# Kernel tuning notes

Hardware: AMD Instinct MI355X
Metric: run time of the kernel (lower is better)

Reference implementation:

```python
import jax, jax.numpy as jnp
import numpy as np
import math

# Dims (match torchaudio Emformer config in init_kwargs)
B, U, D = 4, 512, 80
H, FFN, L = 8, 2048, 12
SEG, LC, RC = 32, 50, 8            # segment_length, left_context, right_context
NUM_SEGS = math.ceil(U / SEG)
RC_LEN = RC * NUM_SEGS
K = RC_LEN + U                      # query/key length = [hard-copied right-context blocks, utterance]
OUT_DIM = 768
EPS = 1e-5
SCALE = (D // H) ** -0.5

def _rc_indices():
    # torchaudio _gen_right_context: per segment, copy the next RC frames; last block is input[T-RC:]
    T = U + RC
    idx = []
    for i in range(NUM_SEGS - 1):
        s = (i + 1) * SEG
        idx.extend(range(s, s + RC))
    idx.extend(range(T - RC, T))
    return np.asarray(idx)

def _attention_mask():
    # torchaudio _gen_attention_mask with use_mem=False. True = disallowed.
    # Rows: all RC blocks (NUM_SEGS * RC rows) first, then utterance queries per segment.
    rc_rows, q_rows = [], []
    for i in range(NUM_SEGS):
        allowed = np.zeros(K, dtype=bool)
        allowed[i * RC:(i + 1) * RC] = True                       # own right-context block
        s = max(i * SEG - LC, 0)
        e = min((i + 1) * SEG, U)
        allowed[RC_LEN + s:RC_LEN + e] = True                     # segment + left context
        rc_rows.append(np.tile(allowed, (RC, 1)))
        q_rows.append(np.tile(allowed, (min(SEG, U - i * SEG), 1)))
    return ~np.concatenate(rc_rows + q_rows, axis=0)              # (K, K)

RC_IDX = _rc_indices()
ATT_MASK = _attention_mask()

def _layer_norm(x, g, b):
    m = jnp.mean(x, axis=-1, keepdims=True)
    v = jnp.var(x, axis=-1, keepdims=True)
    return (x - m) * jax.lax.rsqrt(v + EPS) * g + b

def setup_inputs() -> dict:
    key = jax.random.key(0)
    ks = jax.random.split(key, 8)
    w = lambda k, *s: jax.random.normal(k, s, jnp.float32) * 0.02
    return {
        "mel_input": jax.random.normal(ks[0], (B, U + RC, D), jnp.float32),
        "ln_in_g": jnp.ones((L, D)), "ln_in_b": jnp.zeros((L, D)),
        "Wq": w(ks[1], L, D, D), "bq": jnp.zeros((L, D)),
        "Wkv": w(ks[2], L, 2 * D, D), "bkv": jnp.zeros((L, 2 * D)),
        "Wo": w(ks[3], L, D, D), "bo": jnp.zeros((L, D)),
        "ln_ff_g": jnp.ones((L, D)), "ln_ff_b": jnp.zeros((L, D)),
        "W1": w(ks[4], L, FFN, D), "b1": jnp.zeros((L, FFN)),
        "W2": w(ks[5], L, D, FFN), "b2": jnp.zeros((L, D)),
        "ln_out_g": jnp.ones((L, D)), "ln_out_b": jnp.zeros((L, D)),
        "Wp": w(ks[6], OUT_DIM, D), "bp": jnp.zeros((OUT_DIM,)),
        "lengths": jnp.full((B,), U, dtype=jnp.int32),
    }

def _emformer(mel_input, ln_in_g, ln_in_b, Wq, bq, Wkv, bkv, Wo, bo,
              ln_ff_g, ln_ff_b, W1, b1, W2, b2, ln_out_g, ln_out_b, Wp, bp, lengths):
    att_mask = jnp.asarray(ATT_MASK)
    utt = mel_input[:, :U]                       # (B, U, D)
    rc = mel_input[:, jnp.asarray(RC_IDX)]       # (B, RC_LEN, D)
    # key padding mask over [rc, utterance]: key positions >= lengths + RC_LEN are padded (negative_inf = -1e8)
    pad_mask = jnp.arange(K)[None, :] >= (lengths + RC_LEN)[:, None]   # (B, K)

    def layer(carry, p):
        (lg, lb, wq, bq_, wkv, bkv_, wo, bo_, fg, fb, w1, b1_, w2, b2_, og, ob) = p
        utt, rc = carry
        x = jnp.concatenate([rc, utt], axis=1)   # (B, K, D) -- torchaudio cats [right_context, utterance]
        ln = _layer_norm(x, lg, lb)              # pre-attention LayerNorm
        q = (ln @ wq.T + bq_).reshape(B, K, H, D // H)
        k_, v_ = jnp.split(ln @ wkv.T + bkv_, 2, axis=-1)
        k_ = k_.reshape(B, K, H, D // H)
        v_ = v_.reshape(B, K, H, D // H)
        s = jnp.einsum('bqhd,bkhd->bhqk', q * SCALE, k_).astype(jnp.float32)
        s = jnp.where(att_mask[None, None], -jnp.inf, s)
        s = jnp.where(pad_mask[:, None, None, :], -1e8, s)
        a = jax.nn.softmax(s, axis=-1).astype(x.dtype)
        attn = jnp.einsum('bhqk,bkhd->bqhd', a, v_).reshape(B, K, D)
        res = attn @ wo.T + bo_ + x              # residual with pre-LN input
        ff = _layer_norm(res, fg, fb)            # pos_ff: LN -> Linear -> ReLU -> Linear
        ff = jax.nn.relu(ff @ w1.T + b1_) @ w2.T + b2_
        res = _layer_norm(res + ff, og, ob)      # post LayerNorm
        return (res[:, RC_LEN:], res[:, :RC_LEN]), None

    xs = (ln_in_g, ln_in_b, Wq, bq, Wkv, bkv, Wo, bo, ln_ff_g, ln_ff_b, W1, b1, W2, b2, ln_out_g, ln_out_b)
    (utt, rc), _ = jax.lax.scan(layer, (utt, rc), xs)
    return utt @ Wp.T + bp                       # final projection 80 -> 768

def reference(mel_input, ln_in_g, ln_in_b, Wq, bq, Wkv, bkv, Wo, bo,
              ln_ff_g, ln_ff_b, W1, b1, W2, b2, ln_out_g, ln_out_b, Wp, bp, lengths):
    out = _emformer(mel_input, ln_in_g, ln_in_b, Wq, bq, Wkv, bkv, Wo, bo,
                    ln_ff_g, ln_ff_b, W1, b1, W2, b2, ln_out_g, ln_out_b, Wp, bp, lengths)
    return out, lengths
```

## Files before the change

### kernel.cpp

```cpp
#include <hip/hip_runtime.h>
#include <math.h>

#define BB 4
#define UU 512
#define DD 80
#define HH 8
#define FFND 2048
#define LL 12
#define SEGC 32
#define LCC 50
#define RCC 8
#define NSEG 16
#define RCL 128
#define KK 640
#define ROWS (BB*KK)
#define OUTD 768
#define NSPLIT 8
#define EPSF 1e-5f
#define SCALEF 0.31622776601683794f

typedef __attribute__((ext_vector_type(8))) short bf16x8;
typedef __attribute__((ext_vector_type(4))) float f32x4;

__device__ inline unsigned short f2bf(float f) {
  unsigned int u = __float_as_uint(f);
  u += 0x7fffu + ((u >> 16) & 1u);
  return (unsigned short)(u >> 16);
}

__global__ __launch_bounds__(256) void k_gather(const float* __restrict__ mel,
                                                float* __restrict__ x) {
  int idx = blockIdx.x * 256 + threadIdx.x;
  if (idx >= ROWS * DD) return;
  int d = idx % DD;
  int row = idx / DD;
  int b = row / KK;
  int j = row % KK;
  int pos;
  if (j < RCL) {
    int i = j >> 3, r = j & 7;
    pos = (i < NSEG - 1) ? (i + 1) * SEGC + r : UU + r;
  } else {
    pos = j - RCL;
  }
  x[idx] = mel[(b * (UU + RCC) + pos) * DD + d];
}

__global__ __launch_bounds__(256) void k_cvt(const float* __restrict__ W1,
                                             const float* __restrict__ W2,
                                             unsigned short* __restrict__ o1,
                                             unsigned short* __restrict__ o2) {
  const int NV = (LL * FFND * DD) / 4;
  int t = blockIdx.x * 256 + threadIdx.x;
  const float* src;
  unsigned short* dst;
  int i;
  if (t < NV) { src = W1; dst = o1; i = t; }
  else        { src = W2; dst = o2; i = t - NV; }
  float4 v = reinterpret_cast<const float4*>(src)[i];
  ushort4 r;
  r.x = f2bf(v.x); r.y = f2bf(v.y); r.z = f2bf(v.z); r.w = f2bf(v.w);
  reinterpret_cast<ushort4*>(dst)[i] = r;
}

__global__ __launch_bounds__(256) void k_qkv(
    const float* __restrict__ x, float* __restrict__ qkv,
    const float* __restrict__ Wq, const float* __restrict__ bq,
    const float* __restrict__ Wkv, const float* __restrict__ bkv,
    const float* __restrict__ lg, const float* __restrict__ lb) {
  __shared__ float s_x[32 * 84];
  __shared__ float s_w[80 * 84];
  __shared__ float s_mu[32], s_ri[32];
  int tid = threadIdx.x;
  int r0 = blockIdx.x * 32;
  int ct = blockIdx.y;
  for (int k = 0; k < 3; ++k) {
    int idx = tid + k * 256;
    if (idx < 640) {
      int row = idx / 20, c4 = idx % 20;
      *reinterpret_cast<float4*>(&s_x[row * 84 + c4 * 4]) =
          *reinterpret_cast<const float4*>(&x[(r0 + row) * DD + c4 * 4]);
    }
  }
  const float* Wbase = (ct == 0) ? Wq : (ct == 1 ? Wkv : (Wkv + 80 * DD));
  for (int k = 0; k < 7; ++k) {
    int idx = tid + k * 256;
    if (idx < 1600) {
      int c = idx / 20, d4 = idx % 20;
      *reinterpret_cast<float4*>(&s_w[c * 84 + d4 * 4]) =
          *reinterpret_cast<const float4*>(&Wbase[c * DD + d4 * 4]);
    }
  }
  __syncthreads();
  {
    int rr = tid >> 3, t8 = tid & 7;
    float sm = 0.f, sq = 0.f;
    for (int d = t8 * 10; d < t8 * 10 + 10; ++d) {
      float v = s_x[rr * 84 + d];
      sm += v; sq += v * v;
    }
    for (int m = 4; m >= 1; m >>= 1) {
      sm += __shfl_xor(sm, m, 8);
      sq += __shfl_xor(sq, m, 8);
    }
    if (t8 == 0) {
      float mu = sm * (1.f / DD);
      float var = sq * (1.f / DD) - mu * mu;
      s_mu[rr] = mu;
      s_ri[rr] = rsqrtf(var + EPSF);
    }
  }
  __syncthreads();
  for (int k = 0; k < 10; ++k) {
    int e = tid + k * 256;
    int row = e / 80, d = e % 80;
    s_x[row * 84 + d] = (s_x[row * 84 + d] - s_mu[row]) * s_ri[row] * lg[d] + lb[d];
  }
  __syncthreads();
  int ty = tid >> 4, tx = tid & 15;
  float acc[2][5] = {};
  for (int d4 = 0; d4 < 20; ++d4) {
    float4 a0 = *reinterpret_cast<const float4*>(&s_x[(2 * ty) * 84 + d4 * 4]);
    float4 a1 = *reinterpret_cast<const float4*>(&s_x[(2 * ty + 1) * 84 + d4 * 4]);
#pragma unroll
    for (int j = 0; j < 5; ++j) {
      float4 w = *reinterpret_cast<const float4*>(&s_w[(tx + 16 * j) * 84 + d4 * 4]);
      acc[0][j] += a0.x * w.x + a0.y * w.y + a0.z * w.z + a0.w * w.w;
      acc[1][j] += a1.x * w.x + a1.y * w.y + a1.z * w.z + a1.w * w.w;
    }
  }
  const float* bias = (ct == 0) ? bq : (bkv + (ct == 2 ? 80 : 0));
  for (int i2 = 0; i2 < 2; ++i2)
    for (int j = 0; j < 5; ++j) {
      int c = tx + 16 * j;
      int grow = r0 + 2 * ty + i2;
      qkv[grow * 240 + ct * 80 + c] = acc[i2][j] + bias[c];
    }
}

__global__ __launch_bounds__(256) void k_attn(const float* __restrict__ qkv,
                                              float* __restrict__ attn,
                                              const int* __restrict__ lengths) {
  int i = blockIdx.x, h = blockIdx.y, b = blockIdx.z;
  int tid = threadIdx.x;
  int s = i * SEGC - LCC; if (s < 0) s = 0;
  int e = (i + 1) * SEGC;
  int nk = RCC + (e - s);
  __shared__ float s_k[90 * 10], s_v[90 * 10], s_q[40 * 10];
  __shared__ float s_p[40 * 90], s_kb[90], s_den[40];
  int len = lengths[b];
  if (tid < 90 && tid < nk) {
    int j = tid;
    int kr = (j < RCC) ? i * RCC + j : RCL + s + (j - RCC);
    const float* kp = &qkv[(b * KK + kr) * 240 + 80 + h * 10];
    const float* vp = &qkv[(b * KK + kr) * 240 + 160 + h * 10];
#pragma unroll
    for (int d = 0; d < 10; ++d) { s_k[j * 10 + d] = kp[d]; s_v[j * 10 + d] = vp[d]; }
    s_kb[j] = (kr >= len + RCL) ? -1e8f : 0.f;
  }
  if (tid >= 128 && tid < 168) {
    int j = tid - 128;
    int qr = (j < RCC) ? i * RCC + j : RCL + i * SEGC + (j - RCC);
    const float* qp = &qkv[(b * KK + qr) * 240 + h * 10];
#pragma unroll
    for (int d = 0; d < 10; ++d) s_q[j * 10 + d] = qp[d];
  }
  __syncthreads();
  for (int p = tid; p < 3600; p += 256) {
    int q = p / 90, jk = p % 90;
    float sc = -1e30f;
    if (jk < nk) {
      float dot = 0.f;
#pragma unroll
      for (int d = 0; d < 10; ++d) dot += s_q[q * 10 + d] * s_k[jk * 10 + d];
      sc = dot * SCALEF + s_kb[jk];
    }
    s_p[p] = sc;
  }
  __syncthreads();
  if (tid < 160) {
    int r = tid >> 2, l4 = tid & 3;
    float m = -1e30f;
    for (int kx = l4; kx < 90; kx += 4) m = fmaxf(m, s_p[r * 90 + kx]);
    m = fmaxf(m, __shfl_xor(m, 1, 4));
    m = fmaxf(m, __shfl_xor(m, 2, 4));
    float sum = 0.f;
    for (int kx = l4; kx < 90; kx += 4) {
      float ev = __expf(s_p[r * 90 + kx] - m);
      s_p[r * 90 + kx] = ev;
      sum += ev;
    }
    sum += __shfl_xor(sum, 1, 4);
    sum += __shfl_xor(sum, 2, 4);
    if (l4 == 0) s_den[r] = sum;
  }
  __syncthreads();
  for (int po = tid; po < 400; po += 256) {
    int q = po / 10, d = po % 10;
    float o = 0.f;
    for (int kx = 0; kx < 90; ++kx) o += s_p[q * 90 + kx] * s_v[kx * 10 + d];
    int qr = (q < RCC) ? i * RCC + q : RCL + i * SEGC + (q - RCC);
    attn[(b * KK + qr) * DD + h * 10 + d] = o / s_den[q];
  }
}

__global__ __launch_bounds__(256) void k_oproj(
    const float* __restrict__ attn, const float* __restrict__ Wo,
    const float* __restrict__ bo, const float* __restrict__ x,
    float* __restrict__ res, unsigned short* __restrict__ ffln_bf,
    const float* __restrict__ fg, const float* __restrict__ fb) {
  __shared__ float s_at[16 * 84], s_x2[16 * 84], s_wo[80 * 84];
  int tid = threadIdx.x;
  int r0 = blockIdx.x * 16;
  for (int k = 0; k < 2; ++k) {
    int idx = tid + k * 256;
    if (idx < 320) {
      int row = idx / 20, c4 = idx % 20;
      *reinterpret_cast<float4*>(&s_at[row * 84 + c4 * 4]) =
          *reinterpret_cast<const float4*>(&attn[(r0 + row) * DD + c4 * 4]);
      *reinterpret_cast<float4*>(&s_x2[row * 84 + c4 * 4]) =
          *reinterpret_cast<const float4*>(&x[(r0 + row) * DD + c4 * 4]);
    }
  }
  for (int k = 0; k < 7; ++k) {
    int idx = tid + k * 256;
    if (idx < 1600) {
      int c = idx / 20, d4 = idx % 20;
      *reinterpret_cast<float4*>(&s_wo[c * 84 + d4 * 4]) =
          *reinterpret_cast<const float4*>(&Wo[c * DD + d4 * 4]);
    }
  }
  __syncthreads();
  int r = tid >> 4, tx = tid & 15;
  float acc[5] = {};
  for (int d4 = 0; d4 < 20; ++d4) {
    float4 a = *reinterpret_cast<const float4*>(&s_at[r * 84 + d4 * 4]);
#pragma unroll
    for (int j = 0; j < 5; ++j) {
      float4 w = *reinterpret_cast<const float4*>(&s_wo[(tx + 16 * j) * 84 + d4 * 4]);
      acc[j] += a.x * w.x + a.y * w.y + a.z * w.z + a.w * w.w;
    }
  }
  float val[5];
  float sm = 0.f, sq = 0.f;
#pragma unroll
  for (int j = 0; j < 5; ++j) {
    int c = tx + 16 * j;
    float v = acc[j] + bo[c] + s_x2[r * 84 + c];
    val[j] = v;
    res[(r0 + r) * DD + c] = v;
    sm += v; sq += v * v;
  }
  for (int m = 8; m >= 1; m >>= 1) {
    sm += __shfl_xor(sm, m, 16);
    sq += __shfl_xor(sq, m, 16);
  }
  float mu = sm * (1.f / DD);
  float ri = rsqrtf(sq * (1.f / DD) - mu * mu + EPSF);
#pragma unroll
  for (int j = 0; j < 5; ++j) {
    int c = tx + 16 * j;
    ffln_bf[(r0 + r) * DD + c] = f2bf((val[j] - mu) * ri * fg[c] + fb[c]);
  }
}

__global__ __launch_bounds__(256) void k_ffn(
    const unsigned short* __restrict__ A, const unsigned short* __restrict__ W1,
    const float* __restrict__ b1, const unsigned short* __restrict__ W2,
    float* __restrict__ part) {
  __shared__ unsigned short s_a[64 * 104];
  __shared__ unsigned short s_w1[128 * 104];
  __shared__ unsigned short s_h[64 * 136];
  __shared__ unsigned short s_w2[80 * 136];
  int tid = threadIdx.x;
  int r0 = blockIdx.x * 64;
  int F0 = blockIdx.y * 256;
  int w = tid >> 6, lane = tid & 63;
  int m = lane & 15, q = lane >> 4;

  for (int k = 0; k < 3; ++k) {
    int idx = tid + k * 256;
    if (idx < 640) {
      int row = idx / 10, ch = idx % 10;
      *reinterpret_cast<uint4*>(&s_a[row * 104 + ch * 8]) =
          *reinterpret_cast<const uint4*>(&A[(r0 + row) * DD + ch * 8]);
    }
  }
  if (tid < 128) {
    int row = tid >> 1, half = tid & 1;
    uint4 z = make_uint4(0, 0, 0, 0);
    *reinterpret_cast<uint4*>(&s_a[row * 104 + 80 + half * 8]) = z;
  }
  {
    int fc0 = F0;
    for (int k = 0; k < 5; ++k) {
      int idx = tid + k * 256;
      int row = idx / 10, ch = idx % 10;
      *reinterpret_cast<uint4*>(&s_w1[row * 104 + ch * 8]) =
          *reinterpret_cast<const uint4*>(&W1[(fc0 + row) * DD + ch * 8]);
    }
    {
      int row = tid >> 1, half = tid & 1;
      uint4 z = make_uint4(0, 0, 0, 0);
      *reinterpret_cast<uint4*>(&s_w1[row * 104 + 80 + half * 8]) = z;
    }
    for (int k = 0; k < 5; ++k) {
      int idx = tid + k * 256;
      int row = idx >> 4, ch = idx & 15;
      *reinterpret_cast<uint4*>(&s_w2[row * 136 + ch * 8]) =
          *reinterpret_cast<const uint4*>(&W2[row * FFND + fc0 + ch * 8]);
    }
  }
  __syncthreads();

  f32x4 acc2[5] = {};
  for (int c = 0; c < 2; ++c) {
    int fc0 = F0 + c * 128;
    f32x4 acc1[8] = {};
#pragma unroll
    for (int kk = 0; kk < 3; ++kk) {
      bf16x8 a = *reinterpret_cast<const bf16x8*>(&s_a[(w * 16 + m) * 104 + kk * 32 + q * 8]);
#pragma unroll
      for (int ct = 0; ct < 8; ++ct) {
        bf16x8 b = *reinterpret_cast<const bf16x8*>(&s_w1[(ct * 16 + m) * 104 + kk * 32 + q * 8]);
        acc1[ct] = __builtin_amdgcn_mfma_f32_16x16x32_bf16(a, b, acc1[ct], 0, 0, 0);
      }
    }
#pragma unroll
    for (int ct = 0; ct < 8; ++ct) {
      int col = ct * 16 + m;
      float bias = b1[fc0 + col];
#pragma unroll
      for (int r = 0; r < 4; ++r) {
        int row = w * 16 + q * 4 + r;
        s_h[row * 136 + col] = f2bf(fmaxf(acc1[ct][r] + bias, 0.f));
      }
    }
    __syncthreads();
#pragma unroll
    for (int kk = 0; kk < 4; ++kk) {
      bf16x8 a = *reinterpret_cast<const bf16x8*>(&s_h[(w * 16 + m) * 136 + kk * 32 + q * 8]);
#pragma unroll
      for (int ct = 0; ct < 5; ++ct) {
        bf16x8 b = *reinterpret_cast<const bf16x8*>(&s_w2[(ct * 16 + m) * 136 + kk * 32 + q * 8]);
        acc2[ct] = __builtin_amdgcn_mfma_f32_16x16x32_bf16(a, b, acc2[ct], 0, 0, 0);
      }
    }
    __syncthreads();
    if (c == 0) {
      int fn = F0 + 128;
      for (int k = 0; k < 5; ++k) {
        int idx = tid + k * 256;
        int row = idx / 10, ch = idx % 10;
        *reinterpret_cast<uint4*>(&s_w1[row * 104 + ch * 8]) =
            *reinterpret_cast<const uint4*>(&W1[(fn + row) * DD + ch * 8]);
      }
      for (int k = 0; k < 5; ++k) {
        int idx = tid + k * 256;
        int row = idx >> 4, ch = idx & 15;
        *reinterpret_cast<uint4*>(&s_w2[row * 136 + ch * 8]) =
            *reinterpret_cast<const uint4*>(&W2[row * FFND + fn + ch * 8]);
      }
      __syncthreads();
    }
  }
#pragma unroll
  for (int ct = 0; ct < 5; ++ct)
#pragma unroll
    for (int r = 0; r < 4; ++r) {
      int grow = r0 + w * 16 + q * 4 + r;
      part[blockIdx.y * (ROWS * DD) + grow * DD + ct * 16 + m] = acc2[ct][r];
    }
}

__global__ __launch_bounds__(128) void k_comb(
    const float* __restrict__ part, const float* __restrict__ b2,
    const float* __restrict__ res, float* __restrict__ x,
    const float* __restrict__ og, const float* __restrict__ ob) {
  int row = blockIdx.x;
  int t = threadIdx.x;
  __shared__ float rsum[128], rsq[128];
  float v = 0.f;
  if (t < DD) {
#pragma unroll
    for (int s = 0; s < NSPLIT; ++s) v += part[s * (ROWS * DD) + row * DD + t];
    v += b2[t] + res[row * DD + t];
  }
  rsum[t] = (t < DD) ? v : 0.f;
  rsq[t] = (t < DD) ? v * v : 0.f;
  __syncthreads();
  for (int m2 = 64; m2 >= 1; m2 >>= 1) {
    if (t < m2) { rsum[t] += rsum[t + m2]; rsq[t] += rsq[t + m2]; }
    __syncthreads();
  }
  float mu = rsum[0] * (1.f / DD);
  float ri = rsqrtf(rsq[0] * (1.f / DD) - mu * mu + EPSF);
  if (t < DD) x[row * DD + t] = (v - mu) * ri * og[t] + ob[t];
}

__global__ __launch_bounds__(256) void k_proj(
    const float* __restrict__ x, const float* __restrict__ Wp,
    const float* __restrict__ bp, const int* __restrict__ lengths,
    float* __restrict__ out) {
  __shared__ float s_a[64 * 84], s_w[64 * 84];
  int tid = threadIdx.x;
  int gr0 = blockIdx.x * 64;
  int c0 = blockIdx.y * 64;
  int b = gr0 / UU;
  int u0 = gr0 % UU;
  for (int k = 0; k < 5; ++k) {
    int idx = tid + k * 256;
    int row = idx / 20, c4 = idx % 20;
    *reinterpret_cast<float4*>(&s_a[row * 84 + c4 * 4]) =
        *reinterpret_cast<const float4*>(&x[(b * KK + RCL + u0 + row) * DD + c4 * 4]);
    *reinterpret_cast<float4*>(&s_w[row * 84 + c4 * 4]) =
        *reinterpret_cast<const float4*>(&Wp[(c0 + row) * DD + c4 * 4]);
  }
  __syncthreads();
  int ty = tid >> 4, tx = tid & 15;
  float acc[4][4] = {};
  for (int d4 = 0; d4 < 20; ++d4) {
    float4 a[4], w[4];
#pragma unroll
    for (int i2 = 0; i2 < 4; ++i2)
      a[i2] = *reinterpret_cast<const float4*>(&s_a[(4 * ty + i2) * 84 + d4 * 4]);
#pragma unroll
    for (int j = 0; j < 4; ++j)
      w[j] = *reinterpret_cast<const float4*>(&s_w[(tx + 16 * j) * 84 + d4 * 4]);
#pragma unroll
    for (int i2 = 0; i2 < 4; ++i2)
#pragma unroll
      for (int j = 0; j < 4; ++j)
        acc[i2][j] += a[i2].x * w[j].x + a[i2].y * w[j].y +
                      a[i2].z * w[j].z + a[i2].w * w[j].w;
  }
  for (int i2 = 0; i2 < 4; ++i2)
    for (int j = 0; j < 4; ++j) {
      int c = c0 + tx + 16 * j;
      out[(gr0 + 4 * ty + i2) * OUTD + c] = acc[i2][j] + bp[c];
    }
  if (blockIdx.x == 0 && blockIdx.y == 0 && tid < BB)
    out[BB * UU * OUTD + tid] = (float)lengths[tid];
}

extern "C" void kernel_launch(void* const* d_in, const int* in_sizes, int n_in,
                              void* d_out, int out_size, void* d_ws, size_t ws_size,
                              hipStream_t stream) {
  const float* mel   = (const float*)d_in[0];
  const float* lng   = (const float*)d_in[1];
  const float* lnb   = (const float*)d_in[2];
  const float* Wq    = (const float*)d_in[3];
  const float* bq    = (const float*)d_in[4];
  const float* Wkv   = (const float*)d_in[5];
  const float* bkv   = (const float*)d_in[6];
  const float* Wo    = (const float*)d_in[7];
  const float* bo    = (const float*)d_in[8];
  const float* ffg   = (const float*)d_in[9];
  const float* ffb   = (const float*)d_in[10];
  const float* W1    = (const float*)d_in[11];
  const float* b1    = (const float*)d_in[12];
  const float* W2    = (const float*)d_in[13];
  const float* b2    = (const float*)d_in[14];
  const float* og    = (const float*)d_in[15];
  const float* ob    = (const float*)d_in[16];
  const float* Wp    = (const float*)d_in[17];
  const float* bp    = (const float*)d_in[18];
  const int*   lens  = (const int*)d_in[19];
  float* out = (float*)d_out;

  float* ws   = (float*)d_ws;
  float* x    = ws;
  float* qkv  = x + ROWS * DD;
  float* part = qkv;
  float* attn = qkv + NSPLIT * ROWS * DD;
  float* res  = attn + ROWS * DD;
  unsigned short* ffln_bf = (unsigned short*)(res + ROWS * DD);
  unsigned short* w1bf    = ffln_bf + ROWS * DD;
  unsigned short* w2bf    = w1bf + LL * FFND * DD;

  k_gather<<<(ROWS * DD + 255) / 256, 256, 0, stream>>>(mel, x);
  k_cvt<<<(2 * (LL * FFND * DD) / 4 + 255) / 256, 256, 0, stream>>>(W1, W2, w1bf, w2bf);

  for (int l = 0; l < LL; ++l) {
    const float* lWq  = Wq  + l * DD * DD;
    const float* lbq  = bq  + l * DD;
    const float* lWkv = Wkv + l * 2 * DD * DD;
    const float* lbkv = bkv + l * 2 * DD;
    const float* lWo  = Wo  + l * DD * DD;
    const float* lbo  = bo  + l * DD;
    const unsigned short* lW1 = w1bf + l * FFND * DD;
    const float* lb1  = b1  + l * FFND;
    const unsigned short* lW2 = w2bf + l * FFND * DD;
    const float* lb2  = b2  + l * DD;

    k_qkv<<<dim3(ROWS / 32, 3), 256, 0, stream>>>(
        x, qkv, lWq, lbq, lWkv, lbkv, lng + l * DD, lnb + l * DD);
    k_attn<<<dim3(NSEG, HH, BB), 256, 0, stream>>>(qkv, attn, lens);
    k_oproj<<<ROWS / 16, 256, 0, stream>>>(
        attn, lWo, lbo, x, res, ffln_bf, ffg + l * DD, ffb + l * DD);
    k_ffn<<<dim3(ROWS / 64, NSPLIT), 256, 0, stream>>>(ffln_bf, lW1, lb1, lW2, part);
    k_comb<<<ROWS, 128, 0, stream>>>(part, lb2, res, x, og + l * DD, ob + l * DD);
  }

  k_proj<<<dim3(BB * UU / 64, OUTD / 64), 256, 0, stream>>>(x, Wp, bp, lens, out);
}
```

Before: 616.9 us.

## Fuse attention with output projection and fold FFN combine into next-layer QKV

Attention and the output projection now run in one kernel: each block handles one segment and batch for all heads and keeps the attention output in shared memory, so the separate attn buffer round trip is gone. The FFN split-sum, bias, residual and post-LayerNorm step is folded into the next layer's QKV kernel, and for the last layer into the final projection kernel. This cuts per-layer launches from five to three. In exchange, the attention grid shrinks from 512 small blocks to 64 large blocks with about 110KB of LDS each, and each thread loops serially over four heads, which lowers parallelism in that stage.

```diff
diff --git a/kernel.cpp b/kernel.cpp
--- a/kernel.cpp
+++ b/kernel.cpp
@@ -63,25 +63,21 @@
   reinterpret_cast<ushort4*>(dst)[i] = r;
 }
 
-__global__ __launch_bounds__(256) void k_qkv(
-    const float* __restrict__ x, float* __restrict__ qkv,
+__global__ __launch_bounds__(256) void k_qkvcomb(
+    const float* __restrict__ xin, float* __restrict__ xout,
+    float* __restrict__ qkv,
     const float* __restrict__ Wq, const float* __restrict__ bq,
     const float* __restrict__ Wkv, const float* __restrict__ bkv,
-    const float* __restrict__ lg, const float* __restrict__ lb) {
+    const float* __restrict__ lg, const float* __restrict__ lb,
+    const float* __restrict__ part, const float* __restrict__ res,
+    const float* __restrict__ pb2, const float* __restrict__ pog,
+    const float* __restrict__ pob, int use_comb) {
   __shared__ float s_x[32 * 84];
   __shared__ float s_w[80 * 84];
   __shared__ float s_mu[32], s_ri[32];
   int tid = threadIdx.x;
   int r0 = blockIdx.x * 32;
   int ct = blockIdx.y;
-  for (int k = 0; k < 3; ++k) {
-    int idx = tid + k * 256;
-    if (idx < 640) {
-      int row = idx / 20, c4 = idx % 20;
-      *reinterpret_cast<float4*>(&s_x[row * 84 + c4 * 4]) =
-          *reinterpret_cast<const float4*>(&x[(r0 + row) * DD + c4 * 4]);
-    }
-  }
   const float* Wbase = (ct == 0) ? Wq : (ct == 1 ? Wkv : (Wkv + 80 * DD));
   for (int k = 0; k < 7; ++k) {
     int idx = tid + k * 256;
@@ -91,7 +87,54 @@
           *reinterpret_cast<const float4*>(&Wbase[c * DD + d4 * 4]);
     }
   }
-  __syncthreads();
+  if (!use_comb) {
+    for (int k = 0; k < 3; ++k) {
+      int idx = tid + k * 256;
+      if (idx < 640) {
+        int row = idx / 20, c4 = idx % 20;
+        *reinterpret_cast<float4*>(&s_x[row * 84 + c4 * 4]) =
+            *reinterpret_cast<const float4*>(&xin[(r0 + row) * DD + c4 * 4]);
+      }
+    }
+    __syncthreads();
+  } else {
+    for (int k = 0; k < 10; ++k) {
+      int idx = tid + k * 256;
+      int row = idx / 80, c = idx % 80;
+      int g = r0 + row;
+      float v = pb2[c] + res[g * DD + c];
+#pragma unroll
+      for (int s5 = 0; s5 < NSPLIT; ++s5) v += part[s5 * (ROWS * DD) + g * DD + c];
+      s_x[row * 84 + c] = v;
+    }
+    __syncthreads();
+    {
+      int rr = tid >> 3, t8 = tid & 7;
+      float sm = 0.f, sq = 0.f;
+      for (int d = t8 * 10; d < t8 * 10 + 10; ++d) {
+        float v = s_x[rr * 84 + d];
+        sm += v; sq += v * v;
+      }
+      for (int m = 4; m >= 1; m >>= 1) {
+        sm += __shfl_xor(sm, m, 8);
+        sq += __shfl_xor(sq, m, 8);
+      }
+      if (t8 == 0) {
+        float mu = sm * (1.f / DD);
+        s_mu[rr] = mu;
+        s_ri[rr] = rsqrtf(sq * (1.f / DD) - mu * mu + EPSF);
+      }
+    }
+    __syncthreads();
+    for (int k = 0; k < 10; ++k) {
+      int e = tid + k * 256;
+      int row = e / 80, d = e % 80;
+      float xv = (s_x[row * 84 + d] - s_mu[row]) * s_ri[row] * pog[d] + pob[d];
+      s_x[row * 84 + d] = xv;
+      if (ct == 0) xout[(r0 + row) * DD + d] = xv;
+    }
+    __syncthreads();
+  }
   {
     int rr = tid >> 3, t8 = tid & 7;
     float sm = 0.f, sq = 0.f;
@@ -105,9 +148,8 @@
     }
     if (t8 == 0) {
       float mu = sm * (1.f / DD);
-      float var = sq * (1.f / DD) - mu * mu;
       s_mu[rr] = mu;
-      s_ri[rr] = rsqrtf(var + EPSF);
+      s_ri[rr] = rsqrtf(sq * (1.f / DD) - mu * mu + EPSF);
     }
   }
   __syncthreads();
@@ -138,129 +180,143 @@
     }
 }
 
-__global__ __launch_bounds__(256) void k_attn(const float* __restrict__ qkv,
-                                              float* __restrict__ attn,
-                                              const int* __restrict__ lengths) {
-  int i = blockIdx.x, h = blockIdx.y, b = blockIdx.z;
+__global__ __launch_bounds__(512) void k_attnoproj(
+    const float* __restrict__ qkv, const float* __restrict__ x,
+    const float* __restrict__ Wo, const float* __restrict__ bo,
+    float* __restrict__ res, unsigned short* __restrict__ ffln_bf,
+    const float* __restrict__ fg, const float* __restrict__ fb,
+    const int* __restrict__ lengths) {
+  int i = blockIdx.x, b = blockIdx.y;
   int tid = threadIdx.x;
+  __shared__ float s_k[90 * 80], s_v[90 * 80], s_q[40 * 80];
+  __shared__ float s_ao[40 * 84], s_wo[80 * 84], s_kb[90];
   int s = i * SEGC - LCC; if (s < 0) s = 0;
   int e = (i + 1) * SEGC;
   int nk = RCC + (e - s);
-  __shared__ float s_k[90 * 10], s_v[90 * 10], s_q[40 * 10];
-  __shared__ float s_p[40 * 90], s_kb[90], s_den[40];
   int len = lengths[b];
-  if (tid < 90 && tid < nk) {
-    int j = tid;
+  for (int idx = tid; idx < nk * 20; idx += 512) {
+    int j = idx / 20, c4 = idx % 20;
     int kr = (j < RCC) ? i * RCC + j : RCL + s + (j - RCC);
-    const float* kp = &qkv[(b * KK + kr) * 240 + 80 + h * 10];
-    const float* vp = &qkv[(b * KK + kr) * 240 + 160 + h * 10];
-#pragma unroll
-    for (int d = 0; d < 10; ++d) { s_k[j * 10 + d] = kp[d]; s_v[j * 10 + d] = vp[d]; }
-    s_kb[j] = (kr >= len + RCL) ? -1e8f : 0.f;
-  }
-  if (tid >= 128 && tid < 168) {
-    int j = tid - 128;
+    const float* bp_ = &qkv[(b * KK + kr) * 240];
+    *reinterpret_cast<float4*>(&s_k[j * 80 + c4 * 4]) =
+        *reinterpret_cast<const float4*>(bp_ + 80 + c4 * 4);
+    *reinterpret_cast<float4*>(&s_v[j * 80 + c4 * 4]) =
+        *reinterpret_cast<const float4*>(bp_ + 160 + c4 * 4);
+  }
+  if (tid < 90) {
+    float kb = 0.f;
+    if (tid < nk) {
+      int kr = (tid < RCC) ? i * RCC + tid : RCL + s + (tid - RCC);
+      kb = (kr >= len + RCL) ? -1e8f : 0.f;
+    }
+    s_kb[tid] = kb;
+  }
+  for (int idx = tid; idx < 800; idx += 512) {
+    int j = idx / 20, c4 = idx % 20;
     int qr = (j < RCC) ? i * RCC + j : RCL + i * SEGC + (j - RCC);
-    const float* qp = &qkv[(b * KK + qr) * 240 + h * 10];
-#pragma unroll
-    for (int d = 0; d < 10; ++d) s_q[j * 10 + d] = qp[d];
-  }
-  __syncthreads();
-  for (int p = tid; p < 3600; p += 256) {
-    int q = p / 90, jk = p % 90;
-    float sc = -1e30f;
-    if (jk < nk) {
-      float dot = 0.f;
-#pragma unroll
-      for (int d = 0; d < 10; ++d) dot += s_q[q * 10 + d] * s_k[jk * 10 + d];
-      sc = dot * SCALEF + s_kb[jk];
-    }
-    s_p[p] = sc;
-  }
-  __syncthreads();
-  if (tid < 160) {
-    int r = tid >> 2, l4 = tid & 3;
-    float m = -1e30f;
-    for (int kx = l4; kx < 90; kx += 4) m = fmaxf(m, s_p[r * 90 + kx]);
-    m = fmaxf(m, __shfl_xor(m, 1, 4));
-    m = fmaxf(m, __shfl_xor(m, 2, 4));
-    float sum = 0.f;
-    for (int kx = l4; kx < 90; kx += 4) {
-      float ev = __expf(s_p[r * 90 + kx] - m);
-      s_p[r * 90 + kx] = ev;
-      sum += ev;
-    }
-    sum += __shfl_xor(sum, 1, 4);
-    sum += __shfl_xor(sum, 2, 4);
-    if (l4 == 0) s_den[r] = sum;
-  }
-  __syncthreads();
-  for (int po = tid; po < 400; po += 256) {
-    int q = po / 10, d = po % 10;
-    float o = 0.f;
-    for (int kx = 0; kx < 90; ++kx) o += s_p[q * 90 + kx] * s_v[kx * 10 + d];
-    int qr = (q < RCC) ? i * RCC + q : RCL + i * SEGC + (q - RCC);
-    attn[(b * KK + qr) * DD + h * 10 + d] = o / s_den[q];
-  }
-}
-
-__global__ __launch_bounds__(256) void k_oproj(
-    const float* __restrict__ attn, const float* __restrict__ Wo,
-    const float* __restrict__ bo, const float* __restrict__ x,
-    float* __restrict__ res, unsigned short* __restrict__ ffln_bf,
-    const float* __restrict__ fg, const float* __restrict__ fb) {
-  __shared__ float s_at[16 * 84], s_x2[16 * 84], s_wo[80 * 84];
-  int tid = threadIdx.x;
-  int r0 = blockIdx.x * 16;
-  for (int k = 0; k < 2; ++k) {
-    int idx = tid + k * 256;
-    if (idx < 320) {
-      int row = idx / 20, c4 = idx % 20;
-      *reinterpret_cast<float4*>(&s_at[row * 84 + c4 * 4]) =
-          *reinterpret_cast<const float4*>(&attn[(r0 + row) * DD + c4 * 4]);
-      *reinterpret_cast<float4*>(&s_x2[row * 84 + c4 * 4]) =
-          *reinterpret_cast<const float4*>(&x[(r0 + row) * DD + c4 * 4]);
-    }
-  }
-  for (int k = 0; k < 7; ++k) {
-    int idx = tid + k * 256;
-    if (idx < 1600) {
-      int c = idx / 20, d4 = idx % 20;
-      *reinterpret_cast<float4*>(&s_wo[c * 84 + d4 * 4]) =
-          *reinterpret_cast<const float4*>(&Wo[c * DD + d4 * 4]);
-    }
-  }
-  __syncthreads();
-  int r = tid >> 4, tx = tid & 15;
-  float acc[5] = {};
-  for (int d4 = 0; d4 < 20; ++d4) {
-    float4 a = *reinterpret_cast<const float4*>(&s_at[r * 84 + d4 * 4]);
-#pragma unroll
-    for (int j = 0; j < 5; ++j) {
-      float4 w = *reinterpret_cast<const float4*>(&s_wo[(tx + 16 * j) * 84 + d4 * 4]);
-      acc[j] += a.x * w.x + a.y * w.y + a.z * w.z + a.w * w.w;
-    }
-  }
-  float val[5];
-  float sm = 0.f, sq = 0.f;
-#pragma unroll
-  for (int j = 0; j < 5; ++j) {
-    int c = tx + 16 * j;
-    float v = acc[j] + bo[c] + s_x2[r * 84 + c];
-    val[j] = v;
-    res[(r0 + r) * DD + c] = v;
-    sm += v; sq += v * v;
-  }
-  for (int m = 8; m >= 1; m >>= 1) {
-    sm += __shfl_xor(sm, m, 16);
-    sq += __shfl_xor(sq, m, 16);
-  }
-  float mu = sm * (1.f / DD);
-  float ri = rsqrtf(sq * (1.f / DD) - mu * mu + EPSF);
-#pragma unroll
-  for (int j = 0; j < 5; ++j) {
-    int c = tx + 16 * j;
-    ffln_bf[(r0 + r) * DD + c] = f2bf((val[j] - mu) * ri * fg[c] + fb[c]);
+    *reinterpret_cast<float4*>(&s_q[j * 80 + c4 * 4]) =
+        *reinterpret_cast<const float4*>(&qkv[(b * KK + qr) * 240 + c4 * 4]);
+  }
+  for (int idx = tid; idx < 1600; idx += 512) {
+    int c = idx / 20, d4 = idx % 20;
+    *reinterpret_cast<float4*>(&s_wo[c * 84 + d4 * 4]) =
+        *reinterpret_cast<const float4*>(&Wo[c * DD + d4 * 4]);
+  }
+  __syncthreads();
+  int hg = tid >> 8;
+  int t2 = tid & 255;
+  int q = t2 >> 2, l4 = t2 & 3;
+  if (q < 40) {
+    for (int hi = 0; hi < 4; ++hi) {
+      int h = hg * 4 + hi;
+      float qreg[10];
+#pragma unroll
+      for (int d = 0; d < 10; ++d) qreg[d] = s_q[q * 80 + h * 10 + d];
+      float sc[23];
+#pragma unroll
+      for (int it = 0; it < 23; ++it) {
+        int jk = l4 + it * 4;
+        float v = -1e30f;
+        if (jk < nk) {
+          float dot = 0.f;
+#pragma unroll
+          for (int d = 0; d < 10; ++d) dot += qreg[d] * s_k[jk * 80 + h * 10 + d];
+          v = dot * SCALEF + s_kb[jk];
+        }
+        sc[it] = v;
+      }
+      float m = -1e30f;
+#pragma unroll
+      for (int it = 0; it < 23; ++it) m = fmaxf(m, sc[it]);
+      m = fmaxf(m, __shfl_xor(m, 1, 4));
+      m = fmaxf(m, __shfl_xor(m, 2, 4));
+      float den = 0.f;
+#pragma unroll
+      for (int it = 0; it < 23; ++it) {
+        float p = __expf(sc[it] - m);
+        sc[it] = p; den += p;
+      }
+      den += __shfl_xor(den, 1, 4);
+      den += __shfl_xor(den, 2, 4);
+      float inv = 1.f / den;
+      float o[10] = {};
+#pragma unroll
+      for (int it = 0; it < 23; ++it) {
+        int jk = l4 + it * 4;
+        if (jk < 90) {
+          float p = sc[it];
+#pragma unroll
+          for (int d = 0; d < 10; ++d) o[d] += p * s_v[jk * 80 + h * 10 + d];
+        }
+      }
+#pragma unroll
+      for (int d = 0; d < 10; ++d) {
+        o[d] += __shfl_xor(o[d], 1, 4);
+        o[d] += __shfl_xor(o[d], 2, 4);
+      }
+      if (l4 == 0) {
+#pragma unroll
+        for (int d = 0; d < 10; ++d) s_ao[q * 84 + h * 10 + d] = o[d] * inv;
+      }
+    }
+  }
+  __syncthreads();
+  int r_ = tid >> 4, tx = tid & 15;
+  for (int pass = 0; pass < 2; ++pass) {
+    int row = r_ + pass * 32;
+    if (row < 40) {
+      float acc[5] = {};
+      for (int d4 = 0; d4 < 20; ++d4) {
+        float4 a = *reinterpret_cast<const float4*>(&s_ao[row * 84 + d4 * 4]);
+#pragma unroll
+        for (int j = 0; j < 5; ++j) {
+          float4 w = *reinterpret_cast<const float4*>(&s_wo[(tx + 16 * j) * 84 + d4 * 4]);
+          acc[j] += a.x * w.x + a.y * w.y + a.z * w.z + a.w * w.w;
+        }
+      }
+      int qr = (row < RCC) ? b * KK + i * RCC + row
+                           : b * KK + RCL + i * SEGC + (row - RCC);
+      float val[5];
+      float sm = 0.f, sq = 0.f;
+#pragma unroll
+      for (int j = 0; j < 5; ++j) {
+        int c = tx + 16 * j;
+        float v = acc[j] + bo[c] + x[qr * DD + c];
+        val[j] = v; res[qr * DD + c] = v;
+        sm += v; sq += v * v;
+      }
+      for (int mm = 8; mm >= 1; mm >>= 1) {
+        sm += __shfl_xor(sm, mm, 16);
+        sq += __shfl_xor(sq, mm, 16);
+      }
+      float mu = sm * (1.f / DD);
+      float ri = rsqrtf(sq * (1.f / DD) - mu * mu + EPSF);
+#pragma unroll
+      for (int j = 0; j < 5; ++j) {
+        int c = tx + 16 * j;
+        ffln_bf[qr * DD + c] = f2bf((val[j] - mu) * ri * fg[c] + fb[c]);
+      }
+    }
   }
 }
 
@@ -373,48 +429,57 @@
     }
 }
 
-__global__ __launch_bounds__(128) void k_comb(
-    const float* __restrict__ part, const float* __restrict__ b2,
-    const float* __restrict__ res, float* __restrict__ x,
-    const float* __restrict__ og, const float* __restrict__ ob) {
-  int row = blockIdx.x;
-  int t = threadIdx.x;
-  __shared__ float rsum[128], rsq[128];
-  float v = 0.f;
-  if (t < DD) {
-#pragma unroll
-    for (int s = 0; s < NSPLIT; ++s) v += part[s * (ROWS * DD) + row * DD + t];
-    v += b2[t] + res[row * DD + t];
-  }
-  rsum[t] = (t < DD) ? v : 0.f;
-  rsq[t] = (t < DD) ? v * v : 0.f;
-  __syncthreads();
-  for (int m2 = 64; m2 >= 1; m2 >>= 1) {
-    if (t < m2) { rsum[t] += rsum[t + m2]; rsq[t] += rsq[t + m2]; }
-    __syncthreads();
-  }
-  float mu = rsum[0] * (1.f / DD);
-  float ri = rsqrtf(rsq[0] * (1.f / DD) - mu * mu + EPSF);
-  if (t < DD) x[row * DD + t] = (v - mu) * ri * og[t] + ob[t];
-}
-
-__global__ __launch_bounds__(256) void k_proj(
-    const float* __restrict__ x, const float* __restrict__ Wp,
-    const float* __restrict__ bp, const int* __restrict__ lengths,
-    float* __restrict__ out) {
+__global__ __launch_bounds__(256) void k_projcomb(
+    const float* __restrict__ part, const float* __restrict__ res,
+    const float* __restrict__ pb2, const float* __restrict__ pog,
+    const float* __restrict__ pob,
+    const float* __restrict__ Wp, const float* __restrict__ bp,
+    const int* __restrict__ lengths, float* __restrict__ out) {
   __shared__ float s_a[64 * 84], s_w[64 * 84];
+  __shared__ float s_mu[64], s_ri[64];
   int tid = threadIdx.x;
   int gr0 = blockIdx.x * 64;
   int c0 = blockIdx.y * 64;
   int b = gr0 / UU;
   int u0 = gr0 % UU;
+  for (int k = 0; k < 20; ++k) {
+    int idx = tid + k * 256;
+    int row = idx / 80, c = idx % 80;
+    int g = b * KK + RCL + u0 + row;
+    float v = pb2[c] + res[g * DD + c];
+#pragma unroll
+    for (int s5 = 0; s5 < NSPLIT; ++s5) v += part[s5 * (ROWS * DD) + g * DD + c];
+    s_a[row * 84 + c] = v;
+  }
   for (int k = 0; k < 5; ++k) {
     int idx = tid + k * 256;
     int row = idx / 20, c4 = idx % 20;
-    *reinterpret_cast<float4*>(&s_a[row * 84 + c4 * 4]) =
-        *reinterpret_cast<const float4*>(&x[(b * KK + RCL + u0 + row) * DD + c4 * 4]);
     *reinterpret_cast<float4*>(&s_w[row * 84 + c4 * 4]) =
         *reinterpret_cast<const float4*>(&Wp[(c0 + row) * DD + c4 * 4]);
+  }
+  __syncthreads();
+  for (int p = 0; p < 2; ++p) {
+    int rr = (tid >> 3) + p * 32, t8 = tid & 7;
+    float sm = 0.f, sq = 0.f;
+    for (int d = t8 * 10; d < t8 * 10 + 10; ++d) {
+      float v = s_a[rr * 84 + d];
+      sm += v; sq += v * v;
+    }
+    for (int m = 4; m >= 1; m >>= 1) {
+      sm += __shfl_xor(sm, m, 8);
+      sq += __shfl_xor(sq, m, 8);
+    }
+    if (t8 == 0) {
+      float mu = sm * (1.f / DD);
+      s_mu[rr] = mu;
+      s_ri[rr] = rsqrtf(sq * (1.f / DD) - mu * mu + EPSF);
+    }
+  }
+  __syncthreads();
+  for (int k = 0; k < 20; ++k) {
+    int idx = tid + k * 256;
+    int row = idx / 80, c = idx % 80;
+    s_a[row * 84 + c] = (s_a[row * 84 + c] - s_mu[row]) * s_ri[row] * pog[c] + pob[c];
   }
   __syncthreads();
   int ty = tid >> 4, tx = tid & 15;
@@ -471,9 +536,8 @@
   float* ws   = (float*)d_ws;
   float* x    = ws;
   float* qkv  = x + ROWS * DD;
-  float* part = qkv;
-  float* attn = qkv + NSPLIT * ROWS * DD;
-  float* res  = attn + ROWS * DD;
+  float* part = qkv + ROWS * 240;
+  float* res  = part + NSPLIT * ROWS * DD;
   unsigned short* ffln_bf = (unsigned short*)(res + ROWS * DD);
   unsigned short* w1bf    = ffln_bf + ROWS * DD;
   unsigned short* w2bf    = w1bf + LL * FFND * DD;
@@ -491,16 +555,19 @@
     const unsigned short* lW1 = w1bf + l * FFND * DD;
     const float* lb1  = b1  + l * FFND;
     const unsigned short* lW2 = w2bf + l * FFND * DD;
-    const float* lb2  = b2  + l * DD;
-
-    k_qkv<<<dim3(ROWS / 32, 3), 256, 0, stream>>>(
-        x, qkv, lWq, lbq, lWkv, lbkv, lng + l * DD, lnb + l * DD);
-    k_attn<<<dim3(NSEG, HH, BB), 256, 0, stream>>>(qkv, attn, lens);
-    k_oproj<<<ROWS / 16, 256, 0, stream>>>(
-        attn, lWo, lbo, x, res, ffln_bf, ffg + l * DD, ffb + l * DD);
+
+    const float* pb2 = (l > 0) ? b2 + (l - 1) * DD : b2;
+    const float* pog = (l > 0) ? og + (l - 1) * DD : og;
+    const float* pob = (l > 0) ? ob + (l - 1) * DD : ob;
+
+    k_qkvcomb<<<dim3(ROWS / 32, 3), 256, 0, stream>>>(
+        x, x, qkv, lWq, lbq, lWkv, lbkv, lng + l * DD, lnb + l * DD,
+        part, res, pb2, pog, pob, (l > 0) ? 1 : 0);
+    k_attnoproj<<<dim3(NSEG, BB), 512, 0, stream>>>(
+        qkv, x, lWo, lbo, res, ffln_bf, ffg + l * DD, ffb + l * DD, lens);
     k_ffn<<<dim3(ROWS / 64, NSPLIT), 256, 0, stream>>>(ffln_bf, lW1, lb1, lW2, part);
-    k_comb<<<ROWS, 128, 0, stream>>>(part, lb2, res, x, og + l * DD, ob + l * DD);
-  }
-
-  k_proj<<<dim3(BB * UU / 64, OUTD / 64), 256, 0, stream>>>(x, Wp, bp, lens, out);
-}
+  }
+
+  k_projcomb<<<dim3(BB * UU / 64, OUTD / 64), 256, 0, stream>>>(
+      part, res, b2 + 11 * DD, og + 11 * DD, ob + 11 * DD, Wp, bp, lens, out);
+}
```

Result: slower. 967.2 us (+56.8%).

## Fuse FFN split-K reduction and output LayerNorm into single FFN kernel

Applied to the files above, without the earlier changes.

Removes the 8-way split over the FFN hidden dimension so each block loops over all 2048 hidden units. The second bias, the residual add and the post LayerNorm are applied in the epilogue with shuffle reductions. This eliminates the partial-sum buffer traffic and the separate combine kernel launch. In exchange the grid shrinks from 320 to 40 blocks, which leaves most CUs idle, and each block does eight times more serial work.

```diff
diff --git a/kernel.cpp b/kernel.cpp
--- a/kernel.cpp
+++ b/kernel.cpp
@@ -15,7 +15,6 @@
 #define KK 640
 #define ROWS (BB*KK)
 #define OUTD 768
-#define NSPLIT 8
 #define EPSF 1e-5f
 #define SCALEF 0.31622776601683794f
 
@@ -267,14 +266,15 @@
 __global__ __launch_bounds__(256) void k_ffn(
     const unsigned short* __restrict__ A, const unsigned short* __restrict__ W1,
     const float* __restrict__ b1, const unsigned short* __restrict__ W2,
-    float* __restrict__ part) {
+    const float* __restrict__ b2v, const float* __restrict__ res,
+    float* __restrict__ x,
+    const float* __restrict__ og, const float* __restrict__ ob) {
   __shared__ unsigned short s_a[64 * 104];
   __shared__ unsigned short s_w1[128 * 104];
   __shared__ unsigned short s_h[64 * 136];
   __shared__ unsigned short s_w2[80 * 136];
   int tid = threadIdx.x;
   int r0 = blockIdx.x * 64;
-  int F0 = blockIdx.y * 256;
   int w = tid >> 6, lane = tid & 63;
   int m = lane & 15, q = lane >> 4;
 
@@ -292,30 +292,28 @@
     *reinterpret_cast<uint4*>(&s_a[row * 104 + 80 + half * 8]) = z;
   }
   {
-    int fc0 = F0;
+    int row = tid >> 1, half = tid & 1;
+    uint4 z = make_uint4(0, 0, 0, 0);
+    *reinterpret_cast<uint4*>(&s_w1[row * 104 + 80 + half * 8]) = z;
+  }
+
+  f32x4 acc2[5] = {};
+  for (int c = 0; c < 16; ++c) {
+    int fc0 = c * 128;
+    __syncthreads();
     for (int k = 0; k < 5; ++k) {
       int idx = tid + k * 256;
       int row = idx / 10, ch = idx % 10;
       *reinterpret_cast<uint4*>(&s_w1[row * 104 + ch * 8]) =
           *reinterpret_cast<const uint4*>(&W1[(fc0 + row) * DD + ch * 8]);
     }
-    {
-      int row = tid >> 1, half = tid & 1;
-      uint4 z = make_uint4(0, 0, 0, 0);
-      *reinterpret_cast<uint4*>(&s_w1[row * 104 + 80 + half * 8]) = z;
-    }
     for (int k = 0; k < 5; ++k) {
       int idx = tid + k * 256;
       int row = idx >> 4, ch = idx & 15;
       *reinterpret_cast<uint4*>(&s_w2[row * 136 + ch * 8]) =
           *reinterpret_cast<const uint4*>(&W2[row * FFND + fc0 + ch * 8]);
     }
-  }
-  __syncthreads();
-
-  f32x4 acc2[5] = {};
-  for (int c = 0; c < 2; ++c) {
-    int fc0 = F0 + c * 128;
+    __syncthreads();
     f32x4 acc1[8] = {};
 #pragma unroll
     for (int kk = 0; kk < 3; ++kk) {
@@ -336,7 +334,6 @@
         s_h[row * 136 + col] = f2bf(fmaxf(acc1[ct][r] + bias, 0.f));
       }
     }
-    __syncthreads();
 #pragma unroll
     for (int kk = 0; kk < 4; ++kk) {
       bf16x8 a = *reinterpret_cast<const bf16x8*>(&s_h[(w * 16 + m) * 136 + kk * 32 + q * 8]);
@@ -346,56 +343,40 @@
         acc2[ct] = __builtin_amdgcn_mfma_f32_16x16x32_bf16(a, b, acc2[ct], 0, 0, 0);
       }
     }
-    __syncthreads();
-    if (c == 0) {
-      int fn = F0 + 128;
-      for (int k = 0; k < 5; ++k) {
-        int idx = tid + k * 256;
-        int row = idx / 10, ch = idx % 10;
-        *reinterpret_cast<uint4*>(&s_w1[row * 104 + ch * 8]) =
-            *reinterpret_cast<const uint4*>(&W1[(fn + row) * DD + ch * 8]);
-      }
-      for (int k = 0; k < 5; ++k) {
-        int idx = tid + k * 256;
-        int row = idx >> 4, ch = idx & 15;
-        *reinterpret_cast<uint4*>(&s_w2[row * 136 + ch * 8]) =
-            *reinterpret_cast<const uint4*>(&W2[row * FFND + fn + ch * 8]);
-      }
-      __syncthreads();
-    }
-  }
-#pragma unroll
-  for (int ct = 0; ct < 5; ++ct)
+  }
+  float val[5][4];
+  float sm[4] = {}, sq[4] = {};
+#pragma unroll
+  for (int ct = 0; ct < 5; ++ct) {
+    int col = ct * 16 + m;
+    float bb_ = b2v[col];
 #pragma unroll
     for (int r = 0; r < 4; ++r) {
       int grow = r0 + w * 16 + q * 4 + r;
-      part[blockIdx.y * (ROWS * DD) + grow * DD + ct * 16 + m] = acc2[ct][r];
-    }
-}
-
-__global__ __launch_bounds__(128) void k_comb(
-    const float* __restrict__ part, const float* __restrict__ b2,
-    const float* __restrict__ res, float* __restrict__ x,
-    const float* __restrict__ og, const float* __restrict__ ob) {
-  int row = blockIdx.x;
-  int t = threadIdx.x;
-  __shared__ float rsum[128], rsq[128];
-  float v = 0.f;
-  if (t < DD) {
-#pragma unroll
-    for (int s = 0; s < NSPLIT; ++s) v += part[s * (ROWS * DD) + row * DD + t];
-    v += b2[t] + res[row * DD + t];
-  }
-  rsum[t] = (t < DD) ? v : 0.f;
-  rsq[t] = (t < DD) ? v * v : 0.f;
-  __syncthreads();
-  for (int m2 = 64; m2 >= 1; m2 >>= 1) {
-    if (t < m2) { rsum[t] += rsum[t + m2]; rsq[t] += rsq[t + m2]; }
-    __syncthreads();
-  }
-  float mu = rsum[0] * (1.f / DD);
-  float ri = rsqrtf(rsq[0] * (1.f / DD) - mu * mu + EPSF);
-  if (t < DD) x[row * DD + t] = (v - mu) * ri * og[t] + ob[t];
+      float v = acc2[ct][r] + bb_ + res[grow * DD + col];
+      val[ct][r] = v;
+      sm[r] += v; sq[r] += v * v;
+    }
+  }
+#pragma unroll
+  for (int r = 0; r < 4; ++r) {
+#pragma unroll
+    for (int mm = 8; mm >= 1; mm >>= 1) {
+      sm[r] += __shfl_xor(sm[r], mm, 16);
+      sq[r] += __shfl_xor(sq[r], mm, 16);
+    }
+  }
+#pragma unroll
+  for (int r = 0; r < 4; ++r) {
+    float mu = sm[r] * (1.f / DD);
+    float ri = rsqrtf(sq[r] * (1.f / DD) - mu * mu + EPSF);
+    int grow = r0 + w * 16 + q * 4 + r;
+#pragma unroll
+    for (int ct = 0; ct < 5; ++ct) {
+      int col = ct * 16 + m;
+      x[grow * DD + col] = (val[ct][r] - mu) * ri * og[col] + ob[col];
+    }
+  }
 }
 
 __global__ __launch_bounds__(256) void k_proj(
@@ -471,8 +452,7 @@
   float* ws   = (float*)d_ws;
   float* x    = ws;
   float* qkv  = x + ROWS * DD;
-  float* part = qkv;
-  float* attn = qkv + NSPLIT * ROWS * DD;
+  float* attn = qkv + ROWS * 240;
   float* res  = attn + ROWS * DD;
   unsigned short* ffln_bf = (unsigned short*)(res + ROWS * DD);
   unsigned short* w1bf    = ffln_bf + ROWS * DD;
@@ -498,8 +478,8 @@
     k_attn<<<dim3(NSEG, HH, BB), 256, 0, stream>>>(qkv, attn, lens);
     k_oproj<<<ROWS / 16, 256, 0, stream>>>(
         attn, lWo, lbo, x, res, ffln_bf, ffg + l * DD, ffb + l * DD);
-    k_ffn<<<dim3(ROWS / 64, NSPLIT), 256, 0, stream>>>(ffln_bf, lW1, lb1, lW2, part);
-    k_comb<<<ROWS, 128, 0, stream>>>(part, lb2, res, x, og + l * DD, ob + l * DD);
+    k_ffn<<<ROWS / 64, 256, 0, stream>>>(
+        ffln_bf, lW1, lb1, lW2, lb2, res, x, og + l * DD, ob + l * DD);
   }
 
   k_proj<<<dim3(BB * UU / 64, OUTD / 64), 256, 0, stream>>>(x, Wp, bp, lens, out);
```

Result: slower. 907.0 us (+47.0%).
